# Kernel optimization log

Hardware: AMD Instinct MI355X
Metric: run time of the kernel (lower is better)

The kernel has to match this reference:

```python
import jax, jax.numpy as jnp
import numpy as np

EPS = 1e-6
BASE_CURVATURE = 1.0


def _artanh(x):
    return jnp.arctanh(jnp.clip(x, -1.0 + 1e-5, 1.0 - 1e-5))


def _norm(x):
    return jnp.maximum(jnp.linalg.norm(x, axis=-1, keepdims=True), EPS)


def _logmap0(x, c):
    # Poincare-ball log map at origin
    sc = jnp.sqrt(c)
    n = _norm(x)
    return _artanh(sc * n) * x / (sc * n)


def _expmap0(v, c):
    # Poincare-ball exp map at origin
    sc = jnp.sqrt(c)
    n = _norm(v)
    return jnp.tanh(sc * n) * v / (sc * n)


def _mobius_add(x, y, c):
    x2 = jnp.sum(x * x, axis=-1, keepdims=True)
    y2 = jnp.sum(y * y, axis=-1, keepdims=True)
    xy = jnp.sum(x * y, axis=-1, keepdims=True)
    num = (1.0 + 2.0 * c * xy + c * y2) * x + (1.0 - c * x2) * y
    den = 1.0 + 2.0 * c * xy + (c * c) * x2 * y2
    return num / jnp.maximum(den, EPS)


def _mobius_scalar_mul(t, x, c):
    sc = jnp.sqrt(c)
    n = _norm(x)
    return jnp.tanh(t * _artanh(sc * n)) * x / (sc * n)


def setup_inputs() -> dict:
    key = jax.random.key(0)
    ks = jax.random.split(key, 8)
    B, D_in, D_out, K = 4096, 2048, 2048, 4
    scale_w = np.sqrt(2.0 / (D_in + D_out)) * 0.1
    return {
        "x": jax.random.normal(ks[0], (B, D_in), jnp.float32) * 0.05,
        "weight": jax.random.normal(ks[1], (D_out, D_in), jnp.float32) * scale_w,
        "bias": jax.random.normal(ks[2], (D_out,), jnp.float32) * 0.01,
        "curv_weight": jax.random.normal(ks[3], (1, D_in), jnp.float32) * 0.1,
        "curv_bias": jnp.zeros((1,), jnp.float32),
        "anchors": jax.random.normal(ks[4], (K, D_out), jnp.float32) * 0.3,
        "t_values": jnp.full((K,), 0.5, jnp.float32),
        "anchor_weights": jnp.full((K,), 1.0 / K, jnp.float32),
    }


def reference(x, weight, bias, curv_weight, curv_bias, anchors, t_values, anchor_weights):
    # 1) dynamic curvature prediction: c_i = base_c * softplus(x . w + b), then mean
    logits = x @ curv_weight[0] + curv_bias[0]                 # [B]
    curvatures = BASE_CURVATURE * jax.nn.softplus(logits)      # [B]
    c = jax.lax.stop_gradient(jnp.mean(curvatures))            # scalar (.item() in torch)

    # 2) fused hyperbolic linear: expmap0(logmap0(x) @ W^T + b)
    u = _logmap0(x, c)                                         # [B, D_in]
    h = u @ weight.T + bias                                    # [B, D_out]
    y = _expmap0(h, c)                                         # [B, D_out]

    # 3) geodesic activation: weighted Mobius geodesic toward each anchor
    xe = y[:, None, :]                                         # [B, 1, D]
    a = anchors[None, :, :]                                    # [1, K, D]
    diff = _mobius_add(-xe, a, c)                              # [B, K, D]
    step = _mobius_scalar_mul(t_values[None, :, None], diff, c)
    g = _mobius_add(xe, step, c)                               # [B, K, D]
    w = jax.nn.softmax(anchor_weights)                         # [K]
    return jnp.einsum("bkd,k->bd", g, w)                       # [B, D_out]
```

## Files before the change

kernel.cpp:

```cpp
#include <hip/hip_runtime.h>
#include <stdint.h>

#define B_ROWS 4096
#define D_IN   2048
#define D_OUT  2048
#define KANCH  4

typedef _Float16 half8  __attribute__((ext_vector_type(8)));
typedef _Float16 half4  __attribute__((ext_vector_type(4)));
typedef float    floatx4 __attribute__((ext_vector_type(4)));
typedef const __attribute__((address_space(1))) uint8_t* gptr_t;
typedef __attribute__((address_space(3))) uint8_t* lptr_t;

__device__ __forceinline__ float frcp(float x)   { return __builtin_amdgcn_rcpf(x); }
__device__ __forceinline__ float ftanh(float x)  { float e = __expf(2.f * x); return (e - 1.f) * frcp(e + 1.f); }
__device__ __forceinline__ float fatanh(float z) { return 0.5f * __logf((1.f + z) * frcp(1.f - z)); }

__global__ __launch_bounds__(256) void k_prep(
    const float* __restrict__ x,
    const float* __restrict__ W,
    const float* __restrict__ cw,
    const float* __restrict__ cb,
    const float* __restrict__ bias,
    const float* __restrict__ anchors,
    _Float16* __restrict__ xh,
    _Float16* __restrict__ Wh,
    float* __restrict__ n2x,
    float* __restrict__ scal)
{
    int tid = threadIdx.x;
    if (blockIdx.x < 1024) {
        int w = tid >> 6, lane = tid & 63;
        int row = blockIdx.x * 4 + w;
        const floatx4* xr = (const floatx4*)(x + (size_t)row * D_IN);
        const floatx4* wr = (const floatx4*)cw;
        _Float16* xo = xh + (size_t)row * D_IN;
        float dot = 0.f, ss = 0.f;
#pragma unroll
        for (int i = 0; i < 8; ++i) {
            int idx = i * 64 + lane;
            floatx4 xv = xr[idx];
            floatx4 wv = wr[idx];
#pragma unroll
            for (int j = 0; j < 4; ++j) {
                dot += xv[j] * wv[j];
                ss  += xv[j] * xv[j];
            }
            half4 h = {(_Float16)xv[0], (_Float16)xv[1], (_Float16)xv[2], (_Float16)xv[3]};
            *(half4*)(xo + idx * 4) = h;
        }
#pragma unroll
        for (int off = 32; off; off >>= 1) {
            dot += __shfl_down(dot, off);
            ss  += __shfl_down(ss, off);
        }
        __shared__ float spw[4];
        if (lane == 0) {
            n2x[row] = ss;
            float z = dot + cb[0];
            spw[w] = (z > 20.f) ? z : log1pf(expf(z));
        }
        __syncthreads();
        if (tid == 0)
            atomicAdd(&scal[0], spw[0] + spw[1] + spw[2] + spw[3]);
    } else if (blockIdx.x < 2048) {
        int blk = blockIdx.x - 1024;
        const floatx4* W4 = (const floatx4*)W;
#pragma unroll
        for (int i = 0; i < 4; ++i) {
            int idx = blk * 1024 + i * 256 + tid;
            floatx4 v = W4[idx];
            half4 h = {(_Float16)v[0], (_Float16)v[1], (_Float16)v[2], (_Float16)v[3]};
            *(half4*)(Wh + (size_t)idx * 4) = h;
        }
    } else {
        int w = tid >> 6, lane = tid & 63;
        float bf[8], af[KANCH][8];
        *(floatx4*)(bf)     = *(const floatx4*)(bias + tid * 8);
        *(floatx4*)(bf + 4) = *(const floatx4*)(bias + tid * 8 + 4);
#pragma unroll
        for (int k = 0; k < KANCH; ++k) {
            *(floatx4*)(af[k])     = *(const floatx4*)(anchors + (size_t)k * D_OUT + tid * 8);
            *(floatx4*)(af[k] + 4) = *(const floatx4*)(anchors + (size_t)k * D_OUT + tid * 8 + 4);
        }
        float v[9];
#pragma unroll
        for (int q = 0; q < 9; ++q) v[q] = 0.f;
#pragma unroll
        for (int j = 0; j < 8; ++j) {
            v[0] += bf[j] * bf[j];
#pragma unroll
            for (int k = 0; k < KANCH; ++k) {
                v[1 + k] += bf[j] * af[k][j];
                v[5 + k] += af[k][j] * af[k][j];
            }
        }
#pragma unroll
        for (int off = 32; off; off >>= 1)
#pragma unroll
            for (int q = 0; q < 9; ++q) v[q] += __shfl_down(v[q], off);
        __shared__ float red[4][9];
        if (lane == 0)
#pragma unroll
            for (int q = 0; q < 9; ++q) red[w][q] = v[q];
        __syncthreads();
        if (tid == 0)
#pragma unroll
            for (int q = 0; q < 9; ++q)
                scal[1 + q] = red[0][q] + red[1][q] + red[2][q] + red[3][q];
    }
}

template<int KPB>
__global__ __launch_bounds__(256, 4) void k_gemm(
    const _Float16* __restrict__ A,
    const _Float16* __restrict__ W,
    float* __restrict__ P0,
    float* __restrict__ P1)
{
    __shared__ __align__(16) _Float16 As[128 * 64];
    __shared__ __align__(16) _Float16 Bs[128 * 64];
    int tid = threadIdx.x;
    int lane = tid & 63;
    int w = tid >> 6;
    int wm = (w >> 1) * 64, wn = (w & 1) * 64;
    int bm0 = blockIdx.y * 128, bn0 = blockIdx.x * 128;
    float* P = (blockIdx.z == 0) ? P0 : P1;
    int kbase = blockIdx.z * KPB;

    floatx4 acc[4][4];
#pragma unroll
    for (int mi = 0; mi < 4; ++mi)
#pragma unroll
        for (int ni = 0; ni < 4; ++ni)
            acc[mi][ni] = (floatx4){0.f, 0.f, 0.f, 0.f};

    for (int k0 = 0; k0 < KPB; k0 += 64) {
#pragma unroll
        for (int i = 0; i < 4; ++i) {
            int e = (i * 256 + tid) * 8;
            int r = e >> 6, kk = e & 63;
            __builtin_amdgcn_global_load_lds(
                (gptr_t)(A + (size_t)(bm0 + r) * D_IN + kbase + k0 + kk),
                (lptr_t)(As + e), 16, 0, 0);
            __builtin_amdgcn_global_load_lds(
                (gptr_t)(W + (size_t)(bn0 + r) * D_IN + kbase + k0 + kk),
                (lptr_t)(Bs + e), 16, 0, 0);
        }
        __syncthreads();
#pragma unroll
        for (int ks = 0; ks < 64; ks += 32) {
            int kq = ks + (lane >> 4) * 8;
            half8 afr[4], bfr[4];
#pragma unroll
            for (int mi = 0; mi < 4; ++mi)
                afr[mi] = *(const half8*)(As + (wm + mi * 16 + (lane & 15)) * 64 + kq);
#pragma unroll
            for (int ni = 0; ni < 4; ++ni)
                bfr[ni] = *(const half8*)(Bs + (wn + ni * 16 + (lane & 15)) * 64 + kq);
#pragma unroll
            for (int mi = 0; mi < 4; ++mi)
#pragma unroll
                for (int ni = 0; ni < 4; ++ni)
                    acc[mi][ni] = __builtin_amdgcn_mfma_f32_16x16x32_f16(
                        afr[mi], bfr[ni], acc[mi][ni], 0, 0, 0);
        }
        __syncthreads();
    }
#pragma unroll
    for (int mi = 0; mi < 4; ++mi) {
#pragma unroll
        for (int r = 0; r < 4; ++r) {
            int gm = bm0 + wm + mi * 16 + (lane >> 4) * 4 + r;
#pragma unroll
            for (int ni = 0; ni < 4; ++ni) {
                int gn = bn0 + wn + ni * 16 + (lane & 15);
                P[(size_t)gm * D_OUT + gn] = acc[mi][ni][r];
            }
        }
    }
}

__global__ __launch_bounds__(256) void k_mobius(
    const float* __restrict__ P1,
    const float* __restrict__ bias,
    const float* __restrict__ anchors,
    const float* __restrict__ tv,
    const float* __restrict__ aw,
    const float* __restrict__ n2x,
    const float* __restrict__ scal,
    int split,
    float* __restrict__ out)
{
    int tid = threadIdx.x, w = tid >> 6, lane = tid & 63;
    size_t rowoff = (size_t)blockIdx.x * D_OUT;
    float pf[8], bf[8];
    *(floatx4*)(pf)     = *(const floatx4*)(out + rowoff + tid * 8);
    *(floatx4*)(pf + 4) = *(const floatx4*)(out + rowoff + tid * 8 + 4);
    if (split == 2) {
        floatx4 q0 = *(const floatx4*)(P1 + rowoff + tid * 8);
        floatx4 q1 = *(const floatx4*)(P1 + rowoff + tid * 8 + 4);
#pragma unroll
        for (int j = 0; j < 4; ++j) { pf[j] += q0[j]; pf[4 + j] += q1[j]; }
    }
    *(floatx4*)(bf)     = *(const floatx4*)(bias + tid * 8);
    *(floatx4*)(bf + 4) = *(const floatx4*)(bias + tid * 8 + 4);
    float af[KANCH][8];
#pragma unroll
    for (int k = 0; k < KANCH; ++k) {
        *(floatx4*)(af[k])     = *(const floatx4*)(anchors + (size_t)k * D_OUT + tid * 8);
        *(floatx4*)(af[k] + 4) = *(const floatx4*)(anchors + (size_t)k * D_OUT + tid * 8 + 4);
    }
    float v[6];
#pragma unroll
    for (int q = 0; q < 6; ++q) v[q] = 0.f;
#pragma unroll
    for (int j = 0; j < 8; ++j) {
        v[0] += pf[j] * pf[j];
        v[1] += pf[j] * bf[j];
#pragma unroll
        for (int k = 0; k < KANCH; ++k) v[2 + k] += pf[j] * af[k][j];
    }
#pragma unroll
    for (int off = 32; off; off >>= 1)
#pragma unroll
        for (int q = 0; q < 6; ++q) v[q] += __shfl_down(v[q], off);
    __shared__ float red[4][6];
    __shared__ float cf[2 + KANCH];
    if (lane == 0)
#pragma unroll
        for (int q = 0; q < 6; ++q) red[w][q] = v[q];
    __syncthreads();
    if (w == 0) {
        int k = lane & 3;
        float pp = red[0][0] + red[1][0] + red[2][0] + red[3][0];
        float pb = red[0][1] + red[1][1] + red[2][1] + red[3][1];
        float pa = red[0][2 + k] + red[1][2 + k] + red[2][2 + k] + red[3][2 + k];
        float bb = scal[1];
        float ba = scal[2 + k];
        float aa = scal[6 + k];
        float c = scal[0] * (1.0f / (float)B_ROWS);
        float sc = __builtin_amdgcn_sqrtf(c);
        float nx = fmaxf(__builtin_amdgcn_sqrtf(n2x[blockIdx.x]), 1e-6f);
        float ax = sc * nx;
        float zx = fminf(fmaxf(ax, -1.f + 1e-5f), 1.f - 1e-5f);
        float f = fatanh(zx) * frcp(ax);
        float hh = f * f * pp + 2.f * f * pb + bb;
        float ha = f * pa + ba;
        float ek = __expf(aw[k]);
        float se = ek;
        se += __shfl_xor(se, 1);
        se += __shfl_xor(se, 2);
        float wk = ek * frcp(se);
        float nh = fmaxf(__builtin_amdgcn_sqrtf(hh), 1e-6f);
        float snh = sc * nh;
        float gy = ftanh(snh) * frcp(snh);
        float x2 = gy * gy * hh;
        float B1 = 1.f - c * x2;
        float y2 = aa;
        float dy = gy * ha;
        float A1 = 1.f - 2.f * c * dy + c * y2;
        float den1 = fmaxf(1.f - 2.f * c * dy + c * c * x2 * y2, 1e-6f);
        float rd1 = frcp(den1);
        float al = -A1 * rd1, be = B1 * rd1;
        float nd2 = fmaxf(al * al * x2 + 2.f * al * be * dy + be * be * y2, 0.f);
        float nd = fmaxf(__builtin_amdgcn_sqrtf(nd2), 1e-6f);
        float snd = sc * nd;
        float zc = fminf(fmaxf(snd, -1.f + 1e-5f), 1.f - 1e-5f);
        float s = ftanh(tv[k] * fatanh(zc)) * frcp(snd);
        float y2s = s * s * nd2;
        float xys = s * (al * x2 + be * dy);
        float A2 = 1.f + 2.f * c * xys + c * y2s;
        float den2 = fmaxf(1.f + 2.f * c * xys + c * c * x2 * y2s, 1e-6f);
        float rd2 = frcp(den2);
        float Cy  = (A2 + B1 * s * al) * rd2;
        float Cak = (B1 * s * be) * rd2;
        float chk = wk * Cy;
        chk += __shfl_xor(chk, 1);
        chk += __shfl_xor(chk, 2);
        if (lane == 0) {
            float c0 = gy * chk;
            cf[0] = c0 * f;
            cf[1] = c0;
        }
        if (lane < 4) cf[2 + lane] = wk * Cak;
    }
    __syncthreads();
    float cp = cf[0], cb_ = cf[1];
    float o[8];
#pragma unroll
    for (int j = 0; j < 8; ++j) {
        float val = cp * pf[j] + cb_ * bf[j];
#pragma unroll
        for (int k = 0; k < KANCH; ++k) val += cf[2 + k] * af[k][j];
        o[j] = val;
    }
    *(floatx4*)(out + rowoff + tid * 8)     = *(floatx4*)(o);
    *(floatx4*)(out + rowoff + tid * 8 + 4) = *(floatx4*)(o + 4);
}

extern "C" void kernel_launch(void* const* d_in, const int* in_sizes, int n_in,
                              void* d_out, int out_size, void* d_ws, size_t ws_size,
                              hipStream_t stream) {
    const float* x       = (const float*)d_in[0];
    const float* wt      = (const float*)d_in[1];
    const float* bias    = (const float*)d_in[2];
    const float* cw      = (const float*)d_in[3];
    const float* cb      = (const float*)d_in[4];
    const float* anchors = (const float*)d_in[5];
    const float* tv      = (const float*)d_in[6];
    const float* aw      = (const float*)d_in[7];
    float* out = (float*)d_out;

    _Float16* Wh = (_Float16*)d_ws;
    _Float16* xh = Wh + (size_t)D_OUT * D_IN;
    float* n2x   = (float*)(xh + (size_t)B_ROWS * D_IN);
    float* scal  = n2x + B_ROWS;
    float* P1    = scal + 16;
    size_t need_split = (size_t)((char*)(P1 + (size_t)B_ROWS * D_OUT) - (char*)d_ws);
    int split = (ws_size >= need_split) ? 2 : 1;

    hipMemsetAsync(scal, 0, sizeof(float), stream);
    k_prep<<<2049, 256, 0, stream>>>(x, wt, cw, cb, bias, anchors, xh, Wh, n2x, scal);
    if (split == 2)
        k_gemm<D_IN / 2><<<dim3(D_OUT / 128, B_ROWS / 128, 2), 256, 0, stream>>>(xh, Wh, out, P1);
    else
        k_gemm<D_IN><<<dim3(D_OUT / 128, B_ROWS / 128, 1), 256, 0, stream>>>(xh, Wh, out, P1);
    k_mobius<<<B_ROWS, 256, 0, stream>>>(P1, bias, anchors, tv, aw, n2x, scal, split, out);
}
```

Before: 179.4 us.

## Store split-K GEMM partials in fp16 and replace curvature atomic with per-block partials

The GEMM now writes its split-K partial products as fp16 into dedicated workspace buffers instead of fp32 (one of them previously aliased the output), roughly halving partial-result write and read traffic in the GEMM epilogue and the mobius kernel. The curvature softplus sum is now written per block into a partial array, and every mobius block re-reduces those 1024 partials. This removes the memset launch and the global atomics. The cost is extra precision loss in h from rounding the partials to fp16, plus a small redundant reduction in each mobius block.

```diff
diff --git a/kernel.cpp b/kernel.cpp
--- a/kernel.cpp
+++ b/kernel.cpp
@@ -26,6 +26,7 @@
     _Float16* __restrict__ xh,
     _Float16* __restrict__ Wh,
     float* __restrict__ n2x,
+    float* __restrict__ spart,
     float* __restrict__ scal)
 {
     int tid = threadIdx.x;
@@ -62,7 +63,7 @@
         }
         __syncthreads();
         if (tid == 0)
-            atomicAdd(&scal[0], spw[0] + spw[1] + spw[2] + spw[3]);
+            spart[blockIdx.x] = spw[0] + spw[1] + spw[2] + spw[3];
     } else if (blockIdx.x < 2048) {
         int blk = blockIdx.x - 1024;
         const floatx4* W4 = (const floatx4*)W;
@@ -115,8 +116,8 @@
 __global__ __launch_bounds__(256, 4) void k_gemm(
     const _Float16* __restrict__ A,
     const _Float16* __restrict__ W,
-    float* __restrict__ P0,
-    float* __restrict__ P1)
+    _Float16* __restrict__ P0,
+    _Float16* __restrict__ P1)
 {
     __shared__ __align__(16) _Float16 As[128 * 64];
     __shared__ __align__(16) _Float16 Bs[128 * 64];
@@ -125,7 +126,7 @@
     int w = tid >> 6;
     int wm = (w >> 1) * 64, wn = (w & 1) * 64;
     int bm0 = blockIdx.y * 128, bn0 = blockIdx.x * 128;
-    float* P = (blockIdx.z == 0) ? P0 : P1;
+    _Float16* P = (blockIdx.z == 0) ? P0 : P1;
     int kbase = blockIdx.z * KPB;
 
     floatx4 acc[4][4];
@@ -175,19 +176,21 @@
 #pragma unroll
             for (int ni = 0; ni < 4; ++ni) {
                 int gn = bn0 + wn + ni * 16 + (lane & 15);
-                P[(size_t)gm * D_OUT + gn] = acc[mi][ni][r];
+                P[(size_t)gm * D_OUT + gn] = (_Float16)acc[mi][ni][r];
             }
         }
     }
 }
 
 __global__ __launch_bounds__(256) void k_mobius(
-    const float* __restrict__ P1,
+    const _Float16* __restrict__ P0,
+    const _Float16* __restrict__ P1,
     const float* __restrict__ bias,
     const float* __restrict__ anchors,
     const float* __restrict__ tv,
     const float* __restrict__ aw,
     const float* __restrict__ n2x,
+    const float* __restrict__ spart,
     const float* __restrict__ scal,
     int split,
     float* __restrict__ out)
@@ -195,13 +198,15 @@
     int tid = threadIdx.x, w = tid >> 6, lane = tid & 63;
     size_t rowoff = (size_t)blockIdx.x * D_OUT;
     float pf[8], bf[8];
-    *(floatx4*)(pf)     = *(const floatx4*)(out + rowoff + tid * 8);
-    *(floatx4*)(pf + 4) = *(const floatx4*)(out + rowoff + tid * 8 + 4);
+    {
+        half8 p = *(const half8*)(P0 + rowoff + tid * 8);
+#pragma unroll
+        for (int j = 0; j < 8; ++j) pf[j] = (float)p[j];
+    }
     if (split == 2) {
-        floatx4 q0 = *(const floatx4*)(P1 + rowoff + tid * 8);
-        floatx4 q1 = *(const floatx4*)(P1 + rowoff + tid * 8 + 4);
-#pragma unroll
-        for (int j = 0; j < 4; ++j) { pf[j] += q0[j]; pf[4 + j] += q1[j]; }
+        half8 q = *(const half8*)(P1 + rowoff + tid * 8);
+#pragma unroll
+        for (int j = 0; j < 8; ++j) pf[j] += (float)q[j];
     }
     *(floatx4*)(bf)     = *(const floatx4*)(bias + tid * 8);
     *(floatx4*)(bf + 4) = *(const floatx4*)(bias + tid * 8 + 4);
@@ -211,9 +216,13 @@
         *(floatx4*)(af[k])     = *(const floatx4*)(anchors + (size_t)k * D_OUT + tid * 8);
         *(floatx4*)(af[k] + 4) = *(const floatx4*)(anchors + (size_t)k * D_OUT + tid * 8 + 4);
     }
-    float v[6];
-#pragma unroll
-    for (int q = 0; q < 6; ++q) v[q] = 0.f;
+    float v[7];
+#pragma unroll
+    for (int q = 0; q < 7; ++q) v[q] = 0.f;
+    {
+        floatx4 s4 = ((const floatx4*)spart)[tid];
+        v[6] = s4[0] + s4[1] + s4[2] + s4[3];
+    }
 #pragma unroll
     for (int j = 0; j < 8; ++j) {
         v[0] += pf[j] * pf[j];
@@ -224,22 +233,23 @@
 #pragma unroll
     for (int off = 32; off; off >>= 1)
 #pragma unroll
-        for (int q = 0; q < 6; ++q) v[q] += __shfl_down(v[q], off);
-    __shared__ float red[4][6];
+        for (int q = 0; q < 7; ++q) v[q] += __shfl_down(v[q], off);
+    __shared__ float red[4][7];
     __shared__ float cf[2 + KANCH];
     if (lane == 0)
 #pragma unroll
-        for (int q = 0; q < 6; ++q) red[w][q] = v[q];
+        for (int q = 0; q < 7; ++q) red[w][q] = v[q];
     __syncthreads();
     if (w == 0) {
         int k = lane & 3;
         float pp = red[0][0] + red[1][0] + red[2][0] + red[3][0];
         float pb = red[0][1] + red[1][1] + red[2][1] + red[3][1];
         float pa = red[0][2 + k] + red[1][2 + k] + red[2][2 + k] + red[3][2 + k];
+        float spsum = red[0][6] + red[1][6] + red[2][6] + red[3][6];
         float bb = scal[1];
         float ba = scal[2 + k];
         float aa = scal[6 + k];
-        float c = scal[0] * (1.0f / (float)B_ROWS);
+        float c = spsum * (1.0f / (float)B_ROWS);
         float sc = __builtin_amdgcn_sqrtf(c);
         float nx = fmaxf(__builtin_amdgcn_sqrtf(n2x[blockIdx.x]), 1e-6f);
         float ax = sc * nx;
@@ -315,16 +325,17 @@
     _Float16* Wh = (_Float16*)d_ws;
     _Float16* xh = Wh + (size_t)D_OUT * D_IN;
     float* n2x   = (float*)(xh + (size_t)B_ROWS * D_IN);
-    float* scal  = n2x + B_ROWS;
-    float* P1    = scal + 16;
-    size_t need_split = (size_t)((char*)(P1 + (size_t)B_ROWS * D_OUT) - (char*)d_ws);
-    int split = (ws_size >= need_split) ? 2 : 1;
-
-    hipMemsetAsync(scal, 0, sizeof(float), stream);
-    k_prep<<<2049, 256, 0, stream>>>(x, wt, cw, cb, bias, anchors, xh, Wh, n2x, scal);
+    float* spart = n2x + B_ROWS;
+    float* scal  = spart + 1024;
+    _Float16* P0 = (_Float16*)(scal + 16);
+    _Float16* P1 = P0 + (size_t)B_ROWS * D_OUT;
+    size_t need2 = (size_t)((char*)(P1 + (size_t)B_ROWS * D_OUT) - (char*)d_ws);
+    int split = (ws_size >= need2) ? 2 : 1;
+
+    k_prep<<<2049, 256, 0, stream>>>(x, wt, cw, cb, bias, anchors, xh, Wh, n2x, spart, scal);
     if (split == 2)
-        k_gemm<D_IN / 2><<<dim3(D_OUT / 128, B_ROWS / 128, 2), 256, 0, stream>>>(xh, Wh, out, P1);
+        k_gemm<D_IN / 2><<<dim3(D_OUT / 128, B_ROWS / 128, 2), 256, 0, stream>>>(xh, Wh, P0, P1);
     else
-        k_gemm<D_IN><<<dim3(D_OUT / 128, B_ROWS / 128, 1), 256, 0, stream>>>(xh, Wh, out, P1);
-    k_mobius<<<B_ROWS, 256, 0, stream>>>(P1, bias, anchors, tv, aw, n2x, scal, split, out);
+        k_gemm<D_IN><<<dim3(D_OUT / 128, B_ROWS / 128, 1), 256, 0, stream>>>(xh, Wh, P0, P1);
+    k_mobius<<<B_ROWS, 256, 0, stream>>>(P0, P1, bias, anchors, tv, aw, n2x, spart, scal, split, out);
 }
```

New measurement: 162.5 us. 9.4% less time.
